# Kernel tuning notes

Hardware: AMD Instinct MI355X
Metric: run time of the kernel (lower is better)

The kernel has to match this reference:

```python
import jax, jax.numpy as jnp
import numpy as np

B, S, D, H = 2, 2048, 256, 8
W_STD = 0.02


def setup_inputs() -> dict:
    key = jax.random.key(0)
    ks = jax.random.split(key, 6)
    x = jax.random.normal(ks[0], (B, S, D), jnp.float32)
    e = jax.random.normal(ks[1], (B, S, D), jnp.float32)
    p = jax.random.normal(ks[2], (B, S, D), jnp.float32)
    W_q = W_STD * jax.random.normal(ks[3], (D, D), jnp.float32)
    W_k = W_STD * jax.random.normal(ks[4], (D, D), jnp.float32)
    W_v = W_STD * jax.random.normal(ks[5], (D, D), jnp.float32)
    gamma = jnp.ones((H, 1, 1), jnp.float32)
    return {"x": x, "e": e, "p": p, "W_q": W_q, "W_k": W_k, "W_v": W_v, "gamma": gamma}


def reference(x, e, p, W_q, W_k, W_v, gamma):
    # use_ppe=True: Q = K = p (broadcast to every head), V = e; each head sees
    # the SAME d_embed-wide copy, so project once and broadcast over heads.
    Q = p @ W_q  # [B,S,D]
    K = p @ W_k  # [B,S,D]
    V = e @ W_v  # [B,S,D]
    # squared euclidean distance (torch.cdist(...,p=2)**2), shared across heads
    q2 = jnp.sum(Q * Q, axis=-1)  # [B,S]
    k2 = jnp.sum(K * K, axis=-1)  # [B,S]
    d2 = q2[:, :, None] + k2[:, None, :] - 2.0 * jnp.einsum('bsd,btd->bst', Q, K)
    d2 = jnp.maximum(d2, 0.0)  # [B,S,S]
    # rbf kernel, per-head gamma: krn = exp(-d2 / (-2*gamma + 1e-6))
    krn = -d2[:, None, :, :] / (-2.0 * gamma + 1e-6)  # [B,H,S,S]
    causal = jnp.tril(jnp.ones((S, S), dtype=bool))  # True where attending allowed
    krn = jnp.where(causal, krn, -jnp.inf)
    krn = jnp.exp(krn)  # masked entries -> exp(-inf) = 0
    # dropout layers run in eval mode (identity)
    out = jnp.einsum('bhst,btd->bhsd', krn, V)  # [B,H,S,D]
    return out
```

## Files before the change

### kernel.cpp

```cpp
#include <hip/hip_runtime.h>
#include <hip/hip_bf16.h>


#define BB   2
#define SS   2048
#define DD   256
#define HH   8
#define BSR  (BB*SS)
#define TSPLIT 4

typedef __bf16 bf16_t;
typedef __bf16 bf16x8 __attribute__((ext_vector_type(8)));
typedef float  f32x4  __attribute__((ext_vector_type(4)));

static __device__ __forceinline__ f32x4 mfma16(bf16x8 a, bf16x8 b, f32x4 c) {
    return __builtin_amdgcn_mfma_f32_16x16x32_bf16(a, b, c, 0, 0, 0);
}

__global__ __launch_bounds__(256) void att_wtrans(
    const float* __restrict__ Wq, const float* __restrict__ Wk,
    const float* __restrict__ Wv,
    bf16_t* __restrict__ WFq_h, bf16_t* __restrict__ WFq_l,
    bf16_t* __restrict__ WFk_h, bf16_t* __restrict__ WFk_l,
    bf16_t* __restrict__ WFv, float* __restrict__ q2, float* __restrict__ k2)
{
    __shared__ float tT[64][68];
    const int tid = threadIdx.x;
    if (blockIdx.x == 48) {
        for (int i = tid; i < BSR; i += 256) { q2[i] = 0.f; k2[i] = 0.f; }
        return;
    }
    const int mat = blockIdx.x >> 4;
    const int tl  = blockIdx.x & 15;
    const int tr  = (tl >> 2) * 64, tc = (tl & 3) * 64;
    const float* W = (mat == 0) ? Wq : ((mat == 1) ? Wk : Wv);

#pragma unroll
    for (int i = 0; i < 4; ++i) {
        const int fidx = i * 256 + tid;
        const int r  = fidx >> 4;
        const int c4 = fidx & 15;
        const float4 v = *(const float4*)(W + (size_t)(tr + r) * DD + tc + c4 * 4);
        tT[c4 * 4 + 0][r] = v.x; tT[c4 * 4 + 1][r] = v.y;
        tT[c4 * 4 + 2][r] = v.z; tT[c4 * 4 + 3][r] = v.w;
    }
    __syncthreads();

#pragma unroll
    for (int i = 0; i < 2; ++i) {
        const int uidx  = i * 256 + tid;
        const int chunk = uidx >> 6;
        const int kc_l  = chunk >> 2, c16 = chunk & 3;
        const int u = uidx & 63, m16 = u & 15, quad = u >> 4;
        const float* src = &tT[c16 * 16 + m16][kc_l * 32 + quad * 8];
        const float4 a = *(const float4*)src;
        const float4 bq = *(const float4*)(src + 4);
        const float f[8] = {a.x, a.y, a.z, a.w, bq.x, bq.y, bq.z, bq.w};
        bf16x8 hi, lo;
#pragma unroll
        for (int j = 0; j < 8; ++j) {
            const bf16_t h = (bf16_t)f[j];
            hi[j] = h; lo[j] = (bf16_t)(f[j] - (float)h);
        }
        const int g16 = (tc >> 4) + c16;
        const int kcg = (tr >> 5) + kc_l;
        const size_t off = ((size_t)(g16 * 8 + kcg)) * 512 + (size_t)u * 8;
        if (mat == 0)      { *(bf16x8*)(WFq_h + off) = hi; *(bf16x8*)(WFq_l + off) = lo; }
        else if (mat == 1) { *(bf16x8*)(WFk_h + off) = hi; *(bf16x8*)(WFk_l + off) = lo; }
        else               { *(bf16x8*)(WFv + off)  = hi; }
    }
}

__global__ __launch_bounds__(256, 2) void att_gemm_qkv(
    const float* __restrict__ p, const float* __restrict__ e,
    const bf16_t* __restrict__ WFq_h, const bf16_t* __restrict__ WFq_l,
    const bf16_t* __restrict__ WFk_h, const bf16_t* __restrict__ WFk_l,
    const bf16_t* __restrict__ WFv,
    bf16_t* __restrict__ QFh, bf16_t* __restrict__ QFl,
    bf16_t* __restrict__ KFh, bf16_t* __restrict__ KFl,
    bf16_t* __restrict__ VF, float* __restrict__ q2, float* __restrict__ k2)
{
    __shared__ float pL[16][264];
    __shared__ float eL[16][264];
    __shared__ float fQ[16][68];
    __shared__ float fK[16][68];
    __shared__ float fV[16][68];

    const int tid  = threadIdx.x;
    const int w    = tid >> 6;
    const int lane = tid & 63;
    const int m16  = lane & 15;
    const int quad = lane >> 4;
    const int row0 = (blockIdx.x >> 2) * 16;
    const int nb   = blockIdx.x & 3;

#pragma unroll
    for (int i = 0; i < 4; ++i) {
        const int fidx = i * 256 + tid;
        const int r  = fidx >> 6;
        const int c4 = fidx & 63;
        const float4 pv = *(const float4*)(p + (size_t)(row0 + r) * DD + c4 * 4);
        const float4 ev = *(const float4*)(e + (size_t)(row0 + r) * DD + c4 * 4);
        *(float4*)&pL[r][c4 * 4] = pv;
        *(float4*)&eL[r][c4 * 4] = ev;
    }
    __syncthreads();

    f32x4 aQ = f32x4{0.f, 0.f, 0.f, 0.f};
    f32x4 aK = f32x4{0.f, 0.f, 0.f, 0.f};
    f32x4 aV = f32x4{0.f, 0.f, 0.f, 0.f};

#pragma unroll 2
    for (int kc = 0; kc < 8; ++kc) {
        const float* ps = &pL[m16][kc * 32 + quad * 8];
        const float* es = &eL[m16][kc * 32 + quad * 8];
        const float4 p0 = *(const float4*)ps;
        const float4 p1 = *(const float4*)(ps + 4);
        const float4 e0 = *(const float4*)es;
        const float4 e1 = *(const float4*)(es + 4);
        const float pa[8] = {p0.x, p0.y, p0.z, p0.w, p1.x, p1.y, p1.z, p1.w};
        const float ea[8] = {e0.x, e0.y, e0.z, e0.w, e1.x, e1.y, e1.z, e1.w};
        bf16x8 aph, apl, aeb;
#pragma unroll
        for (int j = 0; j < 8; ++j) {
            const bf16_t h = (bf16_t)pa[j];
            aph[j] = h;
            apl[j] = (bf16_t)(pa[j] - (float)h);
            aeb[j] = (bf16_t)ea[j];
        }
        const size_t wo = ((size_t)((nb * 4 + w) * 8 + kc)) * 512 + (size_t)lane * 8;
        const bf16x8 bqh = *(const bf16x8*)(WFq_h + wo);
        const bf16x8 bql = *(const bf16x8*)(WFq_l + wo);
        const bf16x8 bkh = *(const bf16x8*)(WFk_h + wo);
        const bf16x8 bkl = *(const bf16x8*)(WFk_l + wo);
        const bf16x8 bv  = *(const bf16x8*)(WFv + wo);
        aQ = mfma16(aph, bqh, aQ);
        aQ = mfma16(apl, bqh, aQ);
        aQ = mfma16(aph, bql, aQ);
        aK = mfma16(aph, bkh, aK);
        aK = mfma16(apl, bkh, aK);
        aK = mfma16(aph, bkl, aK);
        aV = mfma16(aeb, bv, aV);
    }

#pragma unroll
    for (int r = 0; r < 4; ++r) {
        const int rl = quad * 4 + r;
        fQ[rl][w * 16 + m16] = aQ[r];
        fK[rl][w * 16 + m16] = aK[r];
        fV[rl][w * 16 + m16] = aV[r];
    }

#pragma unroll
    for (int r = 0; r < 4; ++r) {
        float vq = aQ[r] * aQ[r], vk = aK[r] * aK[r];
#pragma unroll
        for (int off = 8; off >= 1; off >>= 1) {
            vq += __shfl_xor(vq, off);
            vk += __shfl_xor(vk, off);
        }
        if (m16 == 0) {
            atomicAdd(q2 + row0 + quad * 4 + r, vq);
            atomicAdd(k2 + row0 + quad * 4 + r, vk);
        }
    }

    __syncthreads();

    const int b   = row0 >> 11;
    const int sl  = row0 & 2047;
    const int tt  = sl >> 6;
    const int st  = sl >> 5;
    const int w4  = (sl >> 4) & 3;
    const int mt  = (sl >> 4) & 1;
    const int kc2 = (sl >> 5) & 1;
    const int uh  = (sl >> 4) & 1;

    if (w < 2) {
        const int cl = w;
        const float* src = &fQ[m16][cl * 32 + quad * 8];
        const float4 a = *(const float4*)src;
        const float4 c = *(const float4*)(src + 4);
        const float f[8] = {a.x, a.y, a.z, a.w, c.x, c.y, c.z, c.w};
        bf16x8 hi, lo;
#pragma unroll
        for (int j = 0; j < 8; ++j) {
            const bf16_t h = (bf16_t)f[j];
            hi[j] = h; lo[j] = (bf16_t)(f[j] - (float)h);
        }
        const size_t off = ((size_t)(b * 64 + st)) * 8192
                         + (size_t)(mt * 8 + nb * 2 + cl) * 512 + (size_t)lane * 8;
        *(bf16x8*)(QFh + off) = hi; *(bf16x8*)(QFl + off) = lo;
    } else {
        const int cl = w - 2;
        const float* src = &fK[m16][cl * 32 + quad * 8];
        const float4 a = *(const float4*)src;
        const float4 c = *(const float4*)(src + 4);
        const float f[8] = {a.x, a.y, a.z, a.w, c.x, c.y, c.z, c.w};
        bf16x8 hi, lo;
#pragma unroll
        for (int j = 0; j < 8; ++j) {
            const bf16_t h = (bf16_t)f[j];
            hi[j] = h; lo[j] = (bf16_t)(f[j] - (float)h);
        }
        const size_t off = ((size_t)(b * 32 + tt)) * 16384
                         + (size_t)(w4 * 8 + nb * 2 + cl) * 512 + (size_t)lane * 8;
        *(bf16x8*)(KFh + off) = hi; *(bf16x8*)(KFl + off) = lo;
    }

    if (lane < 32) {
        const int nt  = w;
        const int u   = uh * 32 + lane;
        const int tl0 = (lane >> 4) * 8;
        bf16x8 vb;
#pragma unroll
        for (int j = 0; j < 8; ++j)
            vb[j] = (bf16_t)fV[tl0 + j][nt * 16 + (lane & 15)];
        const size_t off = ((size_t)(b * 32 + tt)) * 16384
                         + (size_t)(nb * 8 + kc2 * 4 + nt) * 512 + (size_t)u * 8;
        *(bf16x8*)(VF + off) = vb;
    }
}

__global__ __launch_bounds__(256, 2) void att_flash(
    const bf16_t* __restrict__ QFh, const bf16_t* __restrict__ QFl,
    const bf16_t* __restrict__ KFh, const bf16_t* __restrict__ KFl,
    const bf16_t* __restrict__ VF, const float* __restrict__ q2,
    const float* __restrict__ k2, const float* __restrict__ gamma,
    float* __restrict__ part, float* __restrict__ out)
{
    __shared__ bf16_t Pb[2][32][72];

    const int tid   = threadIdx.x;
    const int pair  = blockIdx.x >> 3;
    const int sub   = blockIdx.x & 7;
    const int split = sub >> 1;
    const int b     = sub & 1;
    const int wave  = tid >> 6;
    const int lane  = tid & 63;
    const int m16   = lane & 15;
    const int quad  = lane >> 4;

    float g[8];
#pragma unroll
    for (int h = 0; h < 8; ++h) g[h] = gamma[h];

    int pb = 0;

    for (int half = 0; half < 2; ++half) {
        const int st = half ? (63 - pair) : pair;
        const int s0 = st * 32;

        bf16x8 aQh[2][8], aQl[2][8];
        const size_t qtile = ((size_t)(b * 64 + st)) * 8192 + (size_t)lane * 8;
#pragma unroll
        for (int mt = 0; mt < 2; ++mt)
#pragma unroll
            for (int kc = 0; kc < 8; ++kc) {
                const size_t base = qtile + (size_t)(mt * 8 + kc) * 512;
                aQh[mt][kc] = *(const bf16x8*)(QFh + base);
                aQl[mt][kc] = *(const bf16x8*)(QFl + base);
            }

        float q2r[2][4];
#pragma unroll
        for (int mt = 0; mt < 2; ++mt)
#pragma unroll
            for (int r = 0; r < 4; ++r)
                q2r[mt][r] = q2[b * SS + s0 + mt * 16 + quad * 4 + r];

        const int n_tiles = (s0 + 31) / 64 + 1;

        for (int h = 0; h < HH; ++h) {
            int rep = 0;
            while (g[rep] != g[h]) ++rep;
            if (rep != h) continue;
            const float cexp = 1.0f / (2.0f * g[h] - 1e-6f);

            f32x4 O[2][4];
#pragma unroll
            for (int mt = 0; mt < 2; ++mt)
#pragma unroll
                for (int nt = 0; nt < 4; ++nt)
                    O[mt][nt] = f32x4{0.f, 0.f, 0.f, 0.f};

            for (int ti = split; ti < n_tiles; ti += TSPLIT) {
                const int t0 = ti * 64;
                const int tg = t0 + wave * 16 + m16;
                const size_t tile = ((size_t)(b * 32 + ti)) * 16384
                                  + (size_t)wave * 4096 + (size_t)lane * 8;

                bf16x8 vf[2][4];
#pragma unroll
                for (int kc2 = 0; kc2 < 2; ++kc2)
#pragma unroll
                    for (int nt = 0; nt < 4; ++nt)
                        vf[kc2][nt] = *(const bf16x8*)(
                            VF + tile + (size_t)(kc2 * 4 + nt) * 512);
                const float k2v = k2[b * SS + tg];

                f32x4 acc0 = f32x4{0.f, 0.f, 0.f, 0.f};
                f32x4 acc1 = f32x4{0.f, 0.f, 0.f, 0.f};
#pragma unroll
                for (int kc = 0; kc < 8; ++kc) {
                    const bf16x8 bh = *(const bf16x8*)(KFh + tile + (size_t)kc * 512);
                    const bf16x8 bl = *(const bf16x8*)(KFl + tile + (size_t)kc * 512);
                    acc0 = mfma16(aQh[0][kc], bh, acc0);
                    acc1 = mfma16(aQh[1][kc], bh, acc1);
                    acc0 = mfma16(aQl[0][kc], bh, acc0);
                    acc1 = mfma16(aQl[1][kc], bh, acc1);
                    acc0 = mfma16(aQh[0][kc], bl, acc0);
                    acc1 = mfma16(aQh[1][kc], bl, acc1);
                }

#pragma unroll
                for (int mt = 0; mt < 2; ++mt) {
#pragma unroll
                    for (int r = 0; r < 4; ++r) {
                        const int sl = mt * 16 + quad * 4 + r;
                        const int sg = s0 + sl;
                        const float dotv = mt ? acc1[r] : acc0[r];
                        float d2 = q2r[mt][r] + k2v - 2.0f * dotv;
                        d2 = fmaxf(d2, 0.0f);
                        const float wgt = (tg <= sg) ? __expf(cexp * d2) : 0.0f;
                        Pb[pb][sl][wave * 16 + m16] = (bf16_t)wgt;
                    }
                }
                __syncthreads();

#pragma unroll
                for (int kc2 = 0; kc2 < 2; ++kc2) {
                    const bf16x8 pa0 = *(const bf16x8*)&Pb[pb][m16][kc2 * 32 + quad * 8];
                    const bf16x8 pa1 = *(const bf16x8*)&Pb[pb][m16 + 16][kc2 * 32 + quad * 8];
#pragma unroll
                    for (int nt = 0; nt < 4; ++nt) {
                        O[0][nt] = mfma16(pa0, vf[kc2][nt], O[0][nt]);
                        O[1][nt] = mfma16(pa1, vf[kc2][nt], O[1][nt]);
                    }
                }
                pb ^= 1;
            }

            float* dst = (split == 0)
                ? out  + (((size_t)b * HH + h) * SS + s0) * DD
                : part + ((((size_t)(split - 1) * BB + b) * HH + h) * SS + s0) * DD;
#pragma unroll
            for (int mt = 0; mt < 2; ++mt)
#pragma unroll
                for (int nt = 0; nt < 4; ++nt)
#pragma unroll
                    for (int r = 0; r < 4; ++r)
                        dst[(size_t)(mt * 16 + quad * 4 + r) * DD
                            + wave * 64 + nt * 16 + m16] = O[mt][nt][r];
        }
    }
}

__global__ __launch_bounds__(256) void att_reduce_bcast(
    const float* __restrict__ gamma, const float* __restrict__ part,
    float* __restrict__ out)
{
    const int j = blockIdx.x * 256 + threadIdx.x;
    const int b = blockIdx.y;
    const int slab = SS * DD / 4;

    float g[8];
#pragma unroll
    for (int h = 0; h < 8; ++h) g[h] = gamma[h];

    const float4* pp = (const float4*)part;
    float4* o4 = (float4*)out;

    float4 repval{0.f, 0.f, 0.f, 0.f};
    int last_rep = -1;
#pragma unroll
    for (int h = 0; h < HH; ++h) {
        int rep = 0;
        while (g[rep] != g[h]) ++rep;
        float4* o = o4 + ((size_t)(b * HH + h)) * slab + j;
        if (rep == h) {
            float4 v = *o;
#pragma unroll
            for (int k = 0; k < 3; ++k) {
                const float4 pv = pp[(((size_t)k * BB + b) * HH + h) * slab + j];
                v.x += pv.x; v.y += pv.y; v.z += pv.z; v.w += pv.w;
            }
            *o = v; repval = v; last_rep = h;
        } else {
            if (last_rep != rep) {
                repval = o4[((size_t)(b * HH + rep)) * slab + j];
                last_rep = rep;
            }
            *o = repval;
        }
    }
}

extern "C" void kernel_launch(void* const* d_in, const int* in_sizes, int n_in,
                              void* d_out, int out_size, void* d_ws, size_t ws_size,
                              hipStream_t stream) {
    (void)in_sizes; (void)n_in; (void)out_size; (void)ws_size;
    const float* e     = (const float*)d_in[1];
    const float* p     = (const float*)d_in[2];
    const float* Wq    = (const float*)d_in[3];
    const float* Wk    = (const float*)d_in[4];
    const float* Wv    = (const float*)d_in[5];
    const float* gamma = (const float*)d_in[6];

    const size_t NROW = (size_t)BSR * DD;
    bf16_t* WFq_h = (bf16_t*)d_ws;
    bf16_t* WFq_l = WFq_h + DD * DD;
    bf16_t* WFk_h = WFq_l + DD * DD;
    bf16_t* WFk_l = WFk_h + DD * DD;
    bf16_t* WFv   = WFk_l + DD * DD;
    float*  q2    = (float*)(WFv + DD * DD);
    float*  k2    = q2 + BSR;
    bf16_t* QFh   = (bf16_t*)(k2 + BSR);
    bf16_t* QFl   = QFh + NROW;
    bf16_t* KFh   = QFl + NROW;
    bf16_t* KFl   = KFh + NROW;
    bf16_t* VF    = KFl + NROW;
    float*  part  = (float*)(VF + NROW);

    float* out = (float*)d_out;

    att_wtrans<<<dim3(49), dim3(256), 0, stream>>>(
        Wq, Wk, Wv, WFq_h, WFq_l, WFk_h, WFk_l, WFv, q2, k2);

    att_gemm_qkv<<<dim3((BSR / 16) * 4), dim3(256), 0, stream>>>(
        p, e, WFq_h, WFq_l, WFk_h, WFk_l, WFv, QFh, QFl, KFh, KFl, VF, q2, k2);

    att_flash<<<dim3(32 * TSPLIT * BB), dim3(256), 0, stream>>>(
        QFh, QFl, KFh, KFl, VF, q2, k2, gamma, part, out);

    att_reduce_bcast<<<dim3(SS * DD / 4 / 256, BB), dim3(256), 0, stream>>>(
        gamma, part, out);
}
```

Before: 136.1 us.

## Fuse split-K reduction and head broadcast into flash kernel via atomic counters

Removes the separate reduce/broadcast kernel. Each flash block now writes its partial output to a workspace slot, bumps a per-(batch, query-tile) atomic counter, and the last arriving block sums the partials and writes every head's output. Split blocks with no key tiles to process now skip the compute. MFMA sections are wrapped in s_setprio raises. This removes one kernel launch and the read-modify-write of the output, in exchange for extra partial-buffer traffic, threadfence and atomic synchronization, and a serialized reduction tail inside the flash kernel.

```diff
diff --git a/kernel.cpp b/kernel.cpp
--- a/kernel.cpp
+++ b/kernel.cpp
@@ -22,12 +22,14 @@
     const float* __restrict__ Wv,
     bf16_t* __restrict__ WFq_h, bf16_t* __restrict__ WFq_l,
     bf16_t* __restrict__ WFk_h, bf16_t* __restrict__ WFk_l,
-    bf16_t* __restrict__ WFv, float* __restrict__ q2, float* __restrict__ k2)
+    bf16_t* __restrict__ WFv, float* __restrict__ q2, float* __restrict__ k2,
+    unsigned* __restrict__ cnt)
 {
     __shared__ float tT[64][68];
     const int tid = threadIdx.x;
     if (blockIdx.x == 48) {
         for (int i = tid; i < BSR; i += 256) { q2[i] = 0.f; k2[i] = 0.f; }
+        for (int i = tid; i < BB * 64; i += 256) cnt[i] = 0u;
         return;
     }
     const int mat = blockIdx.x >> 4;
@@ -227,9 +229,11 @@
     const bf16_t* __restrict__ KFh, const bf16_t* __restrict__ KFl,
     const bf16_t* __restrict__ VF, const float* __restrict__ q2,
     const float* __restrict__ k2, const float* __restrict__ gamma,
-    float* __restrict__ part, float* __restrict__ out)
+    float* __restrict__ part, unsigned* __restrict__ cnt,
+    float* __restrict__ out)
 {
     __shared__ bf16_t Pb[2][32][72];
+    __shared__ int lastFlag;
 
     const int tid   = threadIdx.x;
     const int pair  = blockIdx.x >> 3;
@@ -250,148 +254,149 @@
     for (int half = 0; half < 2; ++half) {
         const int st = half ? (63 - pair) : pair;
         const int s0 = st * 32;
-
-        bf16x8 aQh[2][8], aQl[2][8];
-        const size_t qtile = ((size_t)(b * 64 + st)) * 8192 + (size_t)lane * 8;
-#pragma unroll
-        for (int mt = 0; mt < 2; ++mt)
-#pragma unroll
-            for (int kc = 0; kc < 8; ++kc) {
-                const size_t base = qtile + (size_t)(mt * 8 + kc) * 512;
-                aQh[mt][kc] = *(const bf16x8*)(QFh + base);
-                aQl[mt][kc] = *(const bf16x8*)(QFl + base);
+        const int n_tiles = (s0 + 31) / 64 + 1;
+        const bool active = (split < n_tiles);
+
+        if (active) {
+            bf16x8 aQh[2][8], aQl[2][8];
+            const size_t qtile = ((size_t)(b * 64 + st)) * 8192 + (size_t)lane * 8;
+#pragma unroll
+            for (int mt = 0; mt < 2; ++mt)
+#pragma unroll
+                for (int kc = 0; kc < 8; ++kc) {
+                    const size_t base = qtile + (size_t)(mt * 8 + kc) * 512;
+                    aQh[mt][kc] = *(const bf16x8*)(QFh + base);
+                    aQl[mt][kc] = *(const bf16x8*)(QFl + base);
+                }
+
+            float q2r[2][4];
+#pragma unroll
+            for (int mt = 0; mt < 2; ++mt)
+#pragma unroll
+                for (int r = 0; r < 4; ++r)
+                    q2r[mt][r] = q2[b * SS + s0 + mt * 16 + quad * 4 + r];
+
+            for (int h = 0; h < HH; ++h) {
+                int rep = 0;
+                while (g[rep] != g[h]) ++rep;
+                if (rep != h) continue;
+                const float cexp = 1.0f / (2.0f * g[h] - 1e-6f);
+
+                f32x4 O[2][4];
+#pragma unroll
+                for (int mt = 0; mt < 2; ++mt)
+#pragma unroll
+                    for (int nt = 0; nt < 4; ++nt)
+                        O[mt][nt] = f32x4{0.f, 0.f, 0.f, 0.f};
+
+                for (int ti = split; ti < n_tiles; ti += TSPLIT) {
+                    const int t0 = ti * 64;
+                    const int tg = t0 + wave * 16 + m16;
+                    const size_t tile = ((size_t)(b * 32 + ti)) * 16384
+                                      + (size_t)wave * 4096 + (size_t)lane * 8;
+
+                    bf16x8 vf[2][4];
+#pragma unroll
+                    for (int kc2 = 0; kc2 < 2; ++kc2)
+#pragma unroll
+                        for (int nt = 0; nt < 4; ++nt)
+                            vf[kc2][nt] = *(const bf16x8*)(
+                                VF + tile + (size_t)(kc2 * 4 + nt) * 512);
+                    const float k2v = k2[b * SS + tg];
+
+                    f32x4 acc0 = f32x4{0.f, 0.f, 0.f, 0.f};
+                    f32x4 acc1 = f32x4{0.f, 0.f, 0.f, 0.f};
+                    __builtin_amdgcn_s_setprio(1);
+#pragma unroll
+                    for (int kc = 0; kc < 8; ++kc) {
+                        const bf16x8 bh = *(const bf16x8*)(KFh + tile + (size_t)kc * 512);
+                        const bf16x8 bl = *(const bf16x8*)(KFl + tile + (size_t)kc * 512);
+                        acc0 = mfma16(aQh[0][kc], bh, acc0);
+                        acc1 = mfma16(aQh[1][kc], bh, acc1);
+                        acc0 = mfma16(aQl[0][kc], bh, acc0);
+                        acc1 = mfma16(aQl[1][kc], bh, acc1);
+                        acc0 = mfma16(aQh[0][kc], bl, acc0);
+                        acc1 = mfma16(aQh[1][kc], bl, acc1);
+                    }
+                    __builtin_amdgcn_s_setprio(0);
+
+#pragma unroll
+                    for (int mt = 0; mt < 2; ++mt) {
+#pragma unroll
+                        for (int r = 0; r < 4; ++r) {
+                            const int sl = mt * 16 + quad * 4 + r;
+                            const int sg = s0 + sl;
+                            const float dotv = mt ? acc1[r] : acc0[r];
+                            float d2 = q2r[mt][r] + k2v - 2.0f * dotv;
+                            d2 = fmaxf(d2, 0.0f);
+                            const float wgt = (tg <= sg) ? __expf(cexp * d2) : 0.0f;
+                            Pb[pb][sl][wave * 16 + m16] = (bf16_t)wgt;
+                        }
+                    }
+                    __syncthreads();
+
+                    __builtin_amdgcn_s_setprio(1);
+#pragma unroll
+                    for (int kc2 = 0; kc2 < 2; ++kc2) {
+                        const bf16x8 pa0 = *(const bf16x8*)&Pb[pb][m16][kc2 * 32 + quad * 8];
+                        const bf16x8 pa1 = *(const bf16x8*)&Pb[pb][m16 + 16][kc2 * 32 + quad * 8];
+#pragma unroll
+                        for (int nt = 0; nt < 4; ++nt) {
+                            O[0][nt] = mfma16(pa0, vf[kc2][nt], O[0][nt]);
+                            O[1][nt] = mfma16(pa1, vf[kc2][nt], O[1][nt]);
+                        }
+                    }
+                    __builtin_amdgcn_s_setprio(0);
+                    pb ^= 1;
+                }
+
+                float* dst = part + (((size_t)split * BB + b) * HH + h) * (size_t)SS * DD
+                           + (size_t)s0 * DD;
+#pragma unroll
+                for (int mt = 0; mt < 2; ++mt)
+#pragma unroll
+                    for (int nt = 0; nt < 4; ++nt)
+#pragma unroll
+                        for (int r = 0; r < 4; ++r)
+                            dst[(size_t)(mt * 16 + quad * 4 + r) * DD
+                                + wave * 64 + nt * 16 + m16] = O[mt][nt][r];
             }
-
-        float q2r[2][4];
-#pragma unroll
-        for (int mt = 0; mt < 2; ++mt)
-#pragma unroll
-            for (int r = 0; r < 4; ++r)
-                q2r[mt][r] = q2[b * SS + s0 + mt * 16 + quad * 4 + r];
-
-        const int n_tiles = (s0 + 31) / 64 + 1;
-
-        for (int h = 0; h < HH; ++h) {
-            int rep = 0;
-            while (g[rep] != g[h]) ++rep;
-            if (rep != h) continue;
-            const float cexp = 1.0f / (2.0f * g[h] - 1e-6f);
-
-            f32x4 O[2][4];
-#pragma unroll
-            for (int mt = 0; mt < 2; ++mt)
-#pragma unroll
-                for (int nt = 0; nt < 4; ++nt)
-                    O[mt][nt] = f32x4{0.f, 0.f, 0.f, 0.f};
-
-            for (int ti = split; ti < n_tiles; ti += TSPLIT) {
-                const int t0 = ti * 64;
-                const int tg = t0 + wave * 16 + m16;
-                const size_t tile = ((size_t)(b * 32 + ti)) * 16384
-                                  + (size_t)wave * 4096 + (size_t)lane * 8;
-
-                bf16x8 vf[2][4];
-#pragma unroll
-                for (int kc2 = 0; kc2 < 2; ++kc2)
-#pragma unroll
-                    for (int nt = 0; nt < 4; ++nt)
-                        vf[kc2][nt] = *(const bf16x8*)(
-                            VF + tile + (size_t)(kc2 * 4 + nt) * 512);
-                const float k2v = k2[b * SS + tg];
-
-                f32x4 acc0 = f32x4{0.f, 0.f, 0.f, 0.f};
-                f32x4 acc1 = f32x4{0.f, 0.f, 0.f, 0.f};
-#pragma unroll
-                for (int kc = 0; kc < 8; ++kc) {
-                    const bf16x8 bh = *(const bf16x8*)(KFh + tile + (size_t)kc * 512);
-                    const bf16x8 bl = *(const bf16x8*)(KFl + tile + (size_t)kc * 512);
-                    acc0 = mfma16(aQh[0][kc], bh, acc0);
-                    acc1 = mfma16(aQh[1][kc], bh, acc1);
-                    acc0 = mfma16(aQl[0][kc], bh, acc0);
-                    acc1 = mfma16(aQl[1][kc], bh, acc1);
-                    acc0 = mfma16(aQh[0][kc], bl, acc0);
-                    acc1 = mfma16(aQh[1][kc], bl, acc1);
+        }
+
+        __syncthreads();
+        if (tid == 0) {
+            __threadfence();
+            const unsigned prev = atomicAdd(&cnt[b * 64 + st], 1u);
+            lastFlag = (prev == TSPLIT - 1) ? 1 : 0;
+        }
+        __syncthreads();
+
+        if (lastFlag) {
+            __threadfence();
+            const int kmax = (n_tiles < TSPLIT) ? n_tiles : TSPLIT;
+#pragma unroll
+            for (int j = 0; j < 8; ++j) {
+                const int f4  = j * 256 + tid;
+                const int row = f4 >> 6, c4 = f4 & 63;
+                const size_t rowoff = (size_t)(s0 + row) * DD + (size_t)c4 * 4;
+                float4 s{0.f, 0.f, 0.f, 0.f};
+                int lastr = -1;
+                for (int hq = 0; hq < HH; ++hq) {
+                    int rep = 0;
+                    while (g[rep] != g[hq]) ++rep;
+                    if (rep != lastr) {
+                        s = float4{0.f, 0.f, 0.f, 0.f};
+                        for (int k = 0; k < kmax; ++k) {
+                            const float4 v = *(const float4*)(
+                                part + (((size_t)k * BB + b) * HH + rep) * (size_t)SS * DD
+                                     + rowoff);
+                            s.x += v.x; s.y += v.y; s.z += v.z; s.w += v.w;
+                        }
+                        lastr = rep;
+                    }
+                    *(float4*)(out + ((size_t)(b * HH + hq) * SS) * DD + rowoff) = s;
                 }
-
-#pragma unroll
-                for (int mt = 0; mt < 2; ++mt) {
-#pragma unroll
-                    for (int r = 0; r < 4; ++r) {
-                        const int sl = mt * 16 + quad * 4 + r;
-                        const int sg = s0 + sl;
-                        const float dotv = mt ? acc1[r] : acc0[r];
-                        float d2 = q2r[mt][r] + k2v - 2.0f * dotv;
-                        d2 = fmaxf(d2, 0.0f);
-                        const float wgt = (tg <= sg) ? __expf(cexp * d2) : 0.0f;
-                        Pb[pb][sl][wave * 16 + m16] = (bf16_t)wgt;
-                    }
-                }
-                __syncthreads();
-
-#pragma unroll
-                for (int kc2 = 0; kc2 < 2; ++kc2) {
-                    const bf16x8 pa0 = *(const bf16x8*)&Pb[pb][m16][kc2 * 32 + quad * 8];
-                    const bf16x8 pa1 = *(const bf16x8*)&Pb[pb][m16 + 16][kc2 * 32 + quad * 8];
-#pragma unroll
-                    for (int nt = 0; nt < 4; ++nt) {
-                        O[0][nt] = mfma16(pa0, vf[kc2][nt], O[0][nt]);
-                        O[1][nt] = mfma16(pa1, vf[kc2][nt], O[1][nt]);
-                    }
-                }
-                pb ^= 1;
             }
-
-            float* dst = (split == 0)
-                ? out  + (((size_t)b * HH + h) * SS + s0) * DD
-                : part + ((((size_t)(split - 1) * BB + b) * HH + h) * SS + s0) * DD;
-#pragma unroll
-            for (int mt = 0; mt < 2; ++mt)
-#pragma unroll
-                for (int nt = 0; nt < 4; ++nt)
-#pragma unroll
-                    for (int r = 0; r < 4; ++r)
-                        dst[(size_t)(mt * 16 + quad * 4 + r) * DD
-                            + wave * 64 + nt * 16 + m16] = O[mt][nt][r];
-        }
-    }
-}
-
-__global__ __launch_bounds__(256) void att_reduce_bcast(
-    const float* __restrict__ gamma, const float* __restrict__ part,
-    float* __restrict__ out)
-{
-    const int j = blockIdx.x * 256 + threadIdx.x;
-    const int b = blockIdx.y;
-    const int slab = SS * DD / 4;
-
-    float g[8];
-#pragma unroll
-    for (int h = 0; h < 8; ++h) g[h] = gamma[h];
-
-    const float4* pp = (const float4*)part;
-    float4* o4 = (float4*)out;
-
-    float4 repval{0.f, 0.f, 0.f, 0.f};
-    int last_rep = -1;
-#pragma unroll
-    for (int h = 0; h < HH; ++h) {
-        int rep = 0;
-        while (g[rep] != g[h]) ++rep;
-        float4* o = o4 + ((size_t)(b * HH + h)) * slab + j;
-        if (rep == h) {
-            float4 v = *o;
-#pragma unroll
-            for (int k = 0; k < 3; ++k) {
-                const float4 pv = pp[(((size_t)k * BB + b) * HH + h) * slab + j];
-                v.x += pv.x; v.y += pv.y; v.z += pv.z; v.w += pv.w;
-            }
-            *o = v; repval = v; last_rep = h;
-        } else {
-            if (last_rep != rep) {
-                repval = o4[((size_t)(b * HH + rep)) * slab + j];
-                last_rep = rep;
-            }
-            *o = repval;
         }
     }
 }
@@ -421,18 +426,16 @@
     bf16_t* KFl   = KFh + NROW;
     bf16_t* VF    = KFl + NROW;
     float*  part  = (float*)(VF + NROW);
+    unsigned* cnt = (unsigned*)(part + (size_t)TSPLIT * BB * HH * SS * DD);
 
     float* out = (float*)d_out;
 
     att_wtrans<<<dim3(49), dim3(256), 0, stream>>>(
-        Wq, Wk, Wv, WFq_h, WFq_l, WFk_h, WFk_l, WFv, q2, k2);
+        Wq, Wk, Wv, WFq_h, WFq_l, WFk_h, WFk_l, WFv, q2, k2, cnt);
 
     att_gemm_qkv<<<dim3((BSR / 16) * 4), dim3(256), 0, stream>>>(
         p, e, WFq_h, WFq_l, WFk_h, WFk_l, WFv, QFh, QFl, KFh, KFl, VF, q2, k2);
 
     att_flash<<<dim3(32 * TSPLIT * BB), dim3(256), 0, stream>>>(
-        QFh, QFl, KFh, KFl, VF, q2, k2, gamma, part, out);
-
-    att_reduce_bcast<<<dim3(SS * DD / 4 / 256, BB), dim3(256), 0, stream>>>(
-        gamma, part, out);
+        QFh, QFl, KFh, KFl, VF, q2, k2, gamma, part, cnt, out);
 }
```

Result: slower. 239.6 us (+76.1%).

## Batch four key tiles per flash iteration and widen QKV GEMM blocks

Applied to the files above, without the earlier changes.

The attention kernel now processes four key tiles per loop step, loading their K and V fragments up front and sharing one barrier across them, with the old single-tile loop kept as a tail. The QKV projection kernel has each block compute all four column groups of a 16-row stripe. This reuses the converted p/e fragments and cuts the block count by four. Both kernels drop to launch bounds of one block per CU, so registers can grow at the cost of occupancy.

```diff
diff --git a/kernel.cpp b/kernel.cpp
--- a/kernel.cpp
+++ b/kernel.cpp
@@ -71,7 +71,7 @@
     }
 }
 
-__global__ __launch_bounds__(256, 2) void att_gemm_qkv(
+__global__ __launch_bounds__(256, 1) void att_gemm_qkv(
     const float* __restrict__ p, const float* __restrict__ e,
     const bf16_t* __restrict__ WFq_h, const bf16_t* __restrict__ WFq_l,
     const bf16_t* __restrict__ WFk_h, const bf16_t* __restrict__ WFk_l,
@@ -91,8 +91,7 @@
     const int lane = tid & 63;
     const int m16  = lane & 15;
     const int quad = lane >> 4;
-    const int row0 = (blockIdx.x >> 2) * 16;
-    const int nb   = blockIdx.x & 3;
+    const int row0 = blockIdx.x * 16;
 
 #pragma unroll
     for (int i = 0; i < 4; ++i) {
@@ -106,11 +105,14 @@
     }
     __syncthreads();
 
-    f32x4 aQ = f32x4{0.f, 0.f, 0.f, 0.f};
-    f32x4 aK = f32x4{0.f, 0.f, 0.f, 0.f};
-    f32x4 aV = f32x4{0.f, 0.f, 0.f, 0.f};
-
-#pragma unroll 2
+    f32x4 aQ[4], aK[4], aV[4];
+#pragma unroll
+    for (int nt = 0; nt < 4; ++nt) {
+        aQ[nt] = f32x4{0.f, 0.f, 0.f, 0.f};
+        aK[nt] = f32x4{0.f, 0.f, 0.f, 0.f};
+        aV[nt] = f32x4{0.f, 0.f, 0.f, 0.f};
+    }
+
     for (int kc = 0; kc < 8; ++kc) {
         const float* ps = &pL[m16][kc * 32 + quad * 8];
         const float* es = &eL[m16][kc * 32 + quad * 8];
@@ -128,32 +130,32 @@
             apl[j] = (bf16_t)(pa[j] - (float)h);
             aeb[j] = (bf16_t)ea[j];
         }
-        const size_t wo = ((size_t)((nb * 4 + w) * 8 + kc)) * 512 + (size_t)lane * 8;
-        const bf16x8 bqh = *(const bf16x8*)(WFq_h + wo);
-        const bf16x8 bql = *(const bf16x8*)(WFq_l + wo);
-        const bf16x8 bkh = *(const bf16x8*)(WFk_h + wo);
-        const bf16x8 bkl = *(const bf16x8*)(WFk_l + wo);
-        const bf16x8 bv  = *(const bf16x8*)(WFv + wo);
-        aQ = mfma16(aph, bqh, aQ);
-        aQ = mfma16(apl, bqh, aQ);
-        aQ = mfma16(aph, bql, aQ);
-        aK = mfma16(aph, bkh, aK);
-        aK = mfma16(apl, bkh, aK);
-        aK = mfma16(aph, bkl, aK);
-        aV = mfma16(aeb, bv, aV);
+#pragma unroll
+        for (int nt = 0; nt < 4; ++nt) {
+            const size_t wo = ((size_t)((nt * 4 + w) * 8 + kc)) * 512 + (size_t)lane * 8;
+            const bf16x8 bqh = *(const bf16x8*)(WFq_h + wo);
+            const bf16x8 bql = *(const bf16x8*)(WFq_l + wo);
+            const bf16x8 bkh = *(const bf16x8*)(WFk_h + wo);
+            const bf16x8 bkl = *(const bf16x8*)(WFk_l + wo);
+            const bf16x8 bv  = *(const bf16x8*)(WFv + wo);
+            aQ[nt] = mfma16(aph, bqh, aQ[nt]);
+            aQ[nt] = mfma16(apl, bqh, aQ[nt]);
+            aQ[nt] = mfma16(aph, bql, aQ[nt]);
+            aK[nt] = mfma16(aph, bkh, aK[nt]);
+            aK[nt] = mfma16(apl, bkh, aK[nt]);
+            aK[nt] = mfma16(aph, bkl, aK[nt]);
+            aV[nt] = mfma16(aeb, bv, aV[nt]);
+        }
     }
 
 #pragma unroll
     for (int r = 0; r < 4; ++r) {
-        const int rl = quad * 4 + r;
-        fQ[rl][w * 16 + m16] = aQ[r];
-        fK[rl][w * 16 + m16] = aK[r];
-        fV[rl][w * 16 + m16] = aV[r];
-    }
-
-#pragma unroll
-    for (int r = 0; r < 4; ++r) {
-        float vq = aQ[r] * aQ[r], vk = aK[r] * aK[r];
+        float vq = 0.f, vk = 0.f;
+#pragma unroll
+        for (int nt = 0; nt < 4; ++nt) {
+            vq += aQ[nt][r] * aQ[nt][r];
+            vk += aK[nt][r] * aK[nt][r];
+        }
 #pragma unroll
         for (int off = 8; off >= 1; off >>= 1) {
             vq += __shfl_xor(vq, off);
@@ -164,8 +166,6 @@
             atomicAdd(k2 + row0 + quad * 4 + r, vk);
         }
     }
-
-    __syncthreads();
 
     const int b   = row0 >> 11;
     const int sl  = row0 & 2047;
@@ -176,60 +176,72 @@
     const int kc2 = (sl >> 5) & 1;
     const int uh  = (sl >> 4) & 1;
 
-    if (w < 2) {
-        const int cl = w;
-        const float* src = &fQ[m16][cl * 32 + quad * 8];
-        const float4 a = *(const float4*)src;
-        const float4 c = *(const float4*)(src + 4);
-        const float f[8] = {a.x, a.y, a.z, a.w, c.x, c.y, c.z, c.w};
-        bf16x8 hi, lo;
-#pragma unroll
-        for (int j = 0; j < 8; ++j) {
-            const bf16_t h = (bf16_t)f[j];
-            hi[j] = h; lo[j] = (bf16_t)(f[j] - (float)h);
-        }
-        const size_t off = ((size_t)(b * 64 + st)) * 8192
-                         + (size_t)(mt * 8 + nb * 2 + cl) * 512 + (size_t)lane * 8;
-        *(bf16x8*)(QFh + off) = hi; *(bf16x8*)(QFl + off) = lo;
-    } else {
-        const int cl = w - 2;
-        const float* src = &fK[m16][cl * 32 + quad * 8];
-        const float4 a = *(const float4*)src;
-        const float4 c = *(const float4*)(src + 4);
-        const float f[8] = {a.x, a.y, a.z, a.w, c.x, c.y, c.z, c.w};
-        bf16x8 hi, lo;
-#pragma unroll
-        for (int j = 0; j < 8; ++j) {
-            const bf16_t h = (bf16_t)f[j];
-            hi[j] = h; lo[j] = (bf16_t)(f[j] - (float)h);
-        }
-        const size_t off = ((size_t)(b * 32 + tt)) * 16384
-                         + (size_t)(w4 * 8 + nb * 2 + cl) * 512 + (size_t)lane * 8;
-        *(bf16x8*)(KFh + off) = hi; *(bf16x8*)(KFl + off) = lo;
-    }
-
-    if (lane < 32) {
-        const int nt  = w;
-        const int u   = uh * 32 + lane;
-        const int tl0 = (lane >> 4) * 8;
-        bf16x8 vb;
-#pragma unroll
-        for (int j = 0; j < 8; ++j)
-            vb[j] = (bf16_t)fV[tl0 + j][nt * 16 + (lane & 15)];
-        const size_t off = ((size_t)(b * 32 + tt)) * 16384
-                         + (size_t)(nb * 8 + kc2 * 4 + nt) * 512 + (size_t)u * 8;
-        *(bf16x8*)(VF + off) = vb;
+#pragma unroll
+    for (int nb = 0; nb < 4; ++nb) {
+        __syncthreads();
+#pragma unroll
+        for (int r = 0; r < 4; ++r) {
+            const int rl = quad * 4 + r;
+            fQ[rl][w * 16 + m16] = aQ[nb][r];
+            fK[rl][w * 16 + m16] = aK[nb][r];
+            fV[rl][w * 16 + m16] = aV[nb][r];
+        }
+        __syncthreads();
+
+        if (w < 2) {
+            const int cl = w;
+            const float* src = &fQ[m16][cl * 32 + quad * 8];
+            const float4 a = *(const float4*)src;
+            const float4 c = *(const float4*)(src + 4);
+            const float f[8] = {a.x, a.y, a.z, a.w, c.x, c.y, c.z, c.w};
+            bf16x8 hi, lo;
+#pragma unroll
+            for (int j = 0; j < 8; ++j) {
+                const bf16_t h = (bf16_t)f[j];
+                hi[j] = h; lo[j] = (bf16_t)(f[j] - (float)h);
+            }
+            const size_t off = ((size_t)(b * 64 + st)) * 8192
+                             + (size_t)(mt * 8 + nb * 2 + cl) * 512 + (size_t)lane * 8;
+            *(bf16x8*)(QFh + off) = hi; *(bf16x8*)(QFl + off) = lo;
+        } else {
+            const int cl = w - 2;
+            const float* src = &fK[m16][cl * 32 + quad * 8];
+            const float4 a = *(const float4*)src;
+            const float4 c = *(const float4*)(src + 4);
+            const float f[8] = {a.x, a.y, a.z, a.w, c.x, c.y, c.z, c.w};
+            bf16x8 hi, lo;
+#pragma unroll
+            for (int j = 0; j < 8; ++j) {
+                const bf16_t h = (bf16_t)f[j];
+                hi[j] = h; lo[j] = (bf16_t)(f[j] - (float)h);
+            }
+            const size_t off = ((size_t)(b * 32 + tt)) * 16384
+                             + (size_t)(w4 * 8 + nb * 2 + cl) * 512 + (size_t)lane * 8;
+            *(bf16x8*)(KFh + off) = hi; *(bf16x8*)(KFl + off) = lo;
+        }
+
+        if (lane < 32) {
+            const int u   = uh * 32 + lane;
+            const int tl0 = (lane >> 4) * 8;
+            bf16x8 vb;
+#pragma unroll
+            for (int j = 0; j < 8; ++j)
+                vb[j] = (bf16_t)fV[tl0 + j][w * 16 + (lane & 15)];
+            const size_t off = ((size_t)(b * 32 + tt)) * 16384
+                             + (size_t)(nb * 8 + kc2 * 4 + w) * 512 + (size_t)u * 8;
+            *(bf16x8*)(VF + off) = vb;
+        }
     }
 }
 
-__global__ __launch_bounds__(256, 2) void att_flash(
+__global__ __launch_bounds__(256, 1) void att_flash(
     const bf16_t* __restrict__ QFh, const bf16_t* __restrict__ QFl,
     const bf16_t* __restrict__ KFh, const bf16_t* __restrict__ KFl,
     const bf16_t* __restrict__ VF, const float* __restrict__ q2,
     const float* __restrict__ k2, const float* __restrict__ gamma,
     float* __restrict__ part, float* __restrict__ out)
 {
-    __shared__ bf16_t Pb[2][32][72];
+    __shared__ bf16_t Pb[2][4][32][72];
 
     const int tid   = threadIdx.x;
     const int pair  = blockIdx.x >> 3;
@@ -245,7 +257,7 @@
 #pragma unroll
     for (int h = 0; h < 8; ++h) g[h] = gamma[h];
 
-    int pb = 0;
+    int q = 0;
 
     for (int half = 0; half < 2; ++half) {
         const int st = half ? (63 - pair) : pair;
@@ -284,9 +296,96 @@
                 for (int nt = 0; nt < 4; ++nt)
                     O[mt][nt] = f32x4{0.f, 0.f, 0.f, 0.f};
 
-            for (int ti = split; ti < n_tiles; ti += TSPLIT) {
-                const int t0 = ti * 64;
-                const int tg = t0 + wave * 16 + m16;
+            int ti = split;
+
+            while (ti + 3 * TSPLIT < n_tiles) {
+                int tg[4]; size_t tl[4];
+#pragma unroll
+                for (int k = 0; k < 4; ++k) {
+                    const int tk = ti + k * TSPLIT;
+                    tg[k] = tk * 64 + wave * 16 + m16;
+                    tl[k] = ((size_t)(b * 32 + tk)) * 16384
+                          + (size_t)wave * 4096 + (size_t)lane * 8;
+                }
+
+                bf16x8 vf[4][8];
+#pragma unroll
+                for (int k = 0; k < 4; ++k)
+#pragma unroll
+                    for (int u = 0; u < 8; ++u)
+                        vf[k][u] = *(const bf16x8*)(VF + tl[k] + (size_t)u * 512);
+                float k2v[4];
+#pragma unroll
+                for (int k = 0; k < 4; ++k) k2v[k] = k2[b * SS + tg[k]];
+
+                f32x4 sA[4], sB[4];
+#pragma unroll
+                for (int k = 0; k < 4; ++k) {
+                    sA[k] = f32x4{0.f, 0.f, 0.f, 0.f};
+                    sB[k] = f32x4{0.f, 0.f, 0.f, 0.f};
+                }
+#pragma unroll
+                for (int kc = 0; kc < 8; ++kc) {
+                    bf16x8 bh[4], bl[4];
+#pragma unroll
+                    for (int k = 0; k < 4; ++k) {
+                        bh[k] = *(const bf16x8*)(KFh + tl[k] + (size_t)kc * 512);
+                        bl[k] = *(const bf16x8*)(KFl + tl[k] + (size_t)kc * 512);
+                    }
+#pragma unroll
+                    for (int k = 0; k < 4; ++k) {
+                        sA[k] = mfma16(aQh[0][kc], bh[k], sA[k]);
+                        sB[k] = mfma16(aQh[1][kc], bh[k], sB[k]);
+                    }
+#pragma unroll
+                    for (int k = 0; k < 4; ++k) {
+                        sA[k] = mfma16(aQl[0][kc], bh[k], sA[k]);
+                        sB[k] = mfma16(aQl[1][kc], bh[k], sB[k]);
+                    }
+#pragma unroll
+                    for (int k = 0; k < 4; ++k) {
+                        sA[k] = mfma16(aQh[0][kc], bl[k], sA[k]);
+                        sB[k] = mfma16(aQh[1][kc], bl[k], sB[k]);
+                    }
+                }
+
+#pragma unroll
+                for (int k = 0; k < 4; ++k)
+#pragma unroll
+                    for (int mt = 0; mt < 2; ++mt)
+#pragma unroll
+                        for (int r = 0; r < 4; ++r) {
+                            const int sl = mt * 16 + quad * 4 + r;
+                            const int sg = s0 + sl;
+                            float d2v = q2r[mt][r] + k2v[k]
+                                      - 2.0f * (mt ? sB[k][r] : sA[k][r]);
+                            d2v = fmaxf(d2v, 0.0f);
+                            const float wgt =
+                                (tg[k] <= sg) ? __expf(cexp * d2v) : 0.0f;
+                            Pb[q][k][sl][wave * 16 + m16] = (bf16_t)wgt;
+                        }
+                __syncthreads();
+
+#pragma unroll
+                for (int k = 0; k < 4; ++k)
+#pragma unroll
+                    for (int kc2 = 0; kc2 < 2; ++kc2) {
+                        const bf16x8 pa0 = *(const bf16x8*)
+                            &Pb[q][k][m16][kc2 * 32 + quad * 8];
+                        const bf16x8 pa1 = *(const bf16x8*)
+                            &Pb[q][k][m16 + 16][kc2 * 32 + quad * 8];
+#pragma unroll
+                        for (int nt = 0; nt < 4; ++nt) {
+                            O[0][nt] = mfma16(pa0, vf[k][kc2 * 4 + nt], O[0][nt]);
+                            O[1][nt] = mfma16(pa1, vf[k][kc2 * 4 + nt], O[1][nt]);
+                        }
+                    }
+                q ^= 1;
+                ti += 4 * TSPLIT;
+            }
+
+            while (ti < n_tiles) {
+                const int tg = ti * 64 + wave * 16 + m16;
                 const size_t tile = ((size_t)(b * 32 + ti)) * 16384
                                   + (size_t)wave * 4096 + (size_t)lane * 8;
 
@@ -323,22 +422,23 @@
                         float d2 = q2r[mt][r] + k2v - 2.0f * dotv;
                         d2 = fmaxf(d2, 0.0f);
                         const float wgt = (tg <= sg) ? __expf(cexp * d2) : 0.0f;
-                        Pb[pb][sl][wave * 16 + m16] = (bf16_t)wgt;
+                        Pb[q][0][sl][wave * 16 + m16] = (bf16_t)wgt;
                     }
                 }
                 __syncthreads();
 
 #pragma unroll
                 for (int kc2 = 0; kc2 < 2; ++kc2) {
-                    const bf16x8 pa0 = *(const bf16x8*)&Pb[pb][m16][kc2 * 32 + quad * 8];
-                    const bf16x8 pa1 = *(const bf16x8*)&Pb[pb][m16 + 16][kc2 * 32 + quad * 8];
+                    const bf16x8 pa0 = *(const bf16x8*)&Pb[q][0][m16][kc2 * 32 + quad * 8];
+                    const bf16x8 pa1 = *(const bf16x8*)&Pb[q][0][m16 + 16][kc2 * 32 + quad * 8];
 #pragma unroll
                     for (int nt = 0; nt < 4; ++nt) {
                         O[0][nt] = mfma16(pa0, vf[kc2][nt], O[0][nt]);
                         O[1][nt] = mfma16(pa1, vf[kc2][nt], O[1][nt]);
                     }
                 }
-                pb ^= 1;
+                q ^= 1;
+                ti += TSPLIT;
             }
 
             float* dst = (split == 0)
@@ -381,7 +481,7 @@
         if (rep == h) {
             float4 v = *o;
 #pragma unroll
-            for (int k = 0; k < 3; ++k) {
+            for (int k = 0; k < TSPLIT - 1; ++k) {
                 const float4 pv = pp[(((size_t)k * BB + b) * HH + h) * slab + j];
                 v.x += pv.x; v.y += pv.y; v.z += pv.z; v.w += pv.w;
             }
@@ -427,7 +527,7 @@
     att_wtrans<<<dim3(49), dim3(256), 0, stream>>>(
         Wq, Wk, Wv, WFq_h, WFq_l, WFk_h, WFk_l, WFv, q2, k2);
 
-    att_gemm_qkv<<<dim3((BSR / 16) * 4), dim3(256), 0, stream>>>(
+    att_gemm_qkv<<<dim3(BSR / 16), dim3(256), 0, stream>>>(
         p, e, WFq_h, WFq_l, WFk_h, WFk_l, WFv, QFh, QFl, KFh, KFl, VF, q2, k2);
 
     att_flash<<<dim3(32 * TSPLIT * BB), dim3(256), 0, stream>>>(
```

Measured after the change: 140.5 us. 3.3% more time.

## Replace key-split with 16-row query tiles, drop reduce kernel, write duplicate heads directly

Applied to the files above, without the earlier changes.

The flash kernel now gives each block 16-row query tiles (paired light and heavy under the causal mask) and walks the full key range itself, so the partial-sum buffer and the separate reduce/broadcast kernel are gone. The key loop is unrolled to process four 64-key tiles per barrier, with one LDS buffer per tile. Heads that share a gamma value are written straight from registers. This removes a kernel launch and the extra partial-sum traffic, but per-block register pressure rises (launch bounds cut to 1 wave group per SIMD) and each block runs a longer serial key loop.

```diff
diff --git a/kernel.cpp b/kernel.cpp
--- a/kernel.cpp
+++ b/kernel.cpp
@@ -7,7 +7,6 @@
 #define DD   256
 #define HH   8
 #define BSR  (BB*SS)
-#define TSPLIT 4
 
 typedef __bf16 bf16_t;
 typedef __bf16 bf16x8 __attribute__((ext_vector_type(8)));
@@ -222,20 +221,20 @@
     }
 }
 
-__global__ __launch_bounds__(256, 2) void att_flash(
+__global__ __launch_bounds__(256, 1) void att_flash(
     const bf16_t* __restrict__ QFh, const bf16_t* __restrict__ QFl,
     const bf16_t* __restrict__ KFh, const bf16_t* __restrict__ KFl,
     const bf16_t* __restrict__ VF, const float* __restrict__ q2,
     const float* __restrict__ k2, const float* __restrict__ gamma,
-    float* __restrict__ part, float* __restrict__ out)
+    float* __restrict__ out)
 {
-    __shared__ bf16_t Pb[2][32][72];
+    __shared__ bf16_t Pb[2][4][16][72];
 
     const int tid   = threadIdx.x;
-    const int pair  = blockIdx.x >> 3;
     const int sub   = blockIdx.x & 7;
-    const int split = sub >> 1;
-    const int b     = sub & 1;
+    const int b     = sub >> 2;
+    const int stl   = sub & 3;
+    const int sq    = blockIdx.x >> 3;
     const int wave  = tid >> 6;
     const int lane  = tid & 63;
     const int m16   = lane & 15;
@@ -245,31 +244,27 @@
 #pragma unroll
     for (int h = 0; h < 8; ++h) g[h] = gamma[h];
 
-    int pb = 0;
+    int q = 0;
 
     for (int half = 0; half < 2; ++half) {
-        const int st = half ? (63 - pair) : pair;
-        const int s0 = st * 32;
-
-        bf16x8 aQh[2][8], aQl[2][8];
-        const size_t qtile = ((size_t)(b * 64 + st)) * 8192 + (size_t)lane * 8;
-#pragma unroll
-        for (int mt = 0; mt < 2; ++mt)
-#pragma unroll
-            for (int kc = 0; kc < 8; ++kc) {
-                const size_t base = qtile + (size_t)(mt * 8 + kc) * 512;
-                aQh[mt][kc] = *(const bf16x8*)(QFh + base);
-                aQl[mt][kc] = *(const bf16x8*)(QFl + base);
-            }
-
-        float q2r[2][4];
-#pragma unroll
-        for (int mt = 0; mt < 2; ++mt)
-#pragma unroll
-            for (int r = 0; r < 4; ++r)
-                q2r[mt][r] = q2[b * SS + s0 + mt * 16 + quad * 4 + r];
-
-        const int n_tiles = (s0 + 31) / 64 + 1;
+        const int st = half ? (127 - (sq * 4 + stl)) : (sq * 4 + stl);
+        const int s0 = st * 16;
+
+        bf16x8 aQh[8], aQl[8];
+        const size_t qtile = ((size_t)(b * 64 + (st >> 1))) * 8192
+                           + (size_t)((st & 1) * 8) * 512 + (size_t)lane * 8;
+#pragma unroll
+        for (int kc = 0; kc < 8; ++kc) {
+            aQh[kc] = *(const bf16x8*)(QFh + qtile + (size_t)kc * 512);
+            aQl[kc] = *(const bf16x8*)(QFl + qtile + (size_t)kc * 512);
+        }
+
+        float q2r[4];
+#pragma unroll
+        for (int r = 0; r < 4; ++r)
+            q2r[r] = q2[b * SS + s0 + quad * 4 + r];
+
+        const int n_tiles = st / 4 + 1;
 
         for (int h = 0; h < HH; ++h) {
             int rep = 0;
@@ -277,121 +272,137 @@
             if (rep != h) continue;
             const float cexp = 1.0f / (2.0f * g[h] - 1e-6f);
 
-            f32x4 O[2][4];
-#pragma unroll
-            for (int mt = 0; mt < 2; ++mt)
-#pragma unroll
-                for (int nt = 0; nt < 4; ++nt)
-                    O[mt][nt] = f32x4{0.f, 0.f, 0.f, 0.f};
-
-            for (int ti = split; ti < n_tiles; ti += TSPLIT) {
-                const int t0 = ti * 64;
-                const int tg = t0 + wave * 16 + m16;
+            f32x4 O[4];
+#pragma unroll
+            for (int nt = 0; nt < 4; ++nt)
+                O[nt] = f32x4{0.f, 0.f, 0.f, 0.f};
+
+            int ti = 0;
+
+            while (ti + 3 < n_tiles) {
+                int tg[4]; size_t tl[4];
+#pragma unroll
+                for (int k = 0; k < 4; ++k) {
+                    tg[k] = (ti + k) * 64 + wave * 16 + m16;
+                    tl[k] = ((size_t)(b * 32 + ti + k)) * 16384
+                          + (size_t)wave * 4096 + (size_t)lane * 8;
+                }
+
+                bf16x8 vf[4][8];
+#pragma unroll
+                for (int k = 0; k < 4; ++k)
+#pragma unroll
+                    for (int u = 0; u < 8; ++u)
+                        vf[k][u] = *(const bf16x8*)(VF + tl[k] + (size_t)u * 512);
+                float k2v[4];
+#pragma unroll
+                for (int k = 0; k < 4; ++k) k2v[k] = k2[b * SS + tg[k]];
+
+                f32x4 sA[4];
+#pragma unroll
+                for (int k = 0; k < 4; ++k) sA[k] = f32x4{0.f, 0.f, 0.f, 0.f};
+#pragma unroll
+                for (int kc = 0; kc < 8; ++kc) {
+                    bf16x8 bh[4], bl[4];
+#pragma unroll
+                    for (int k = 0; k < 4; ++k) {
+                        bh[k] = *(const bf16x8*)(KFh + tl[k] + (size_t)kc * 512);
+                        bl[k] = *(const bf16x8*)(KFl + tl[k] + (size_t)kc * 512);
+                    }
+#pragma unroll
+                    for (int k = 0; k < 4; ++k)
+                        sA[k] = mfma16(aQh[kc], bh[k], sA[k]);
+#pragma unroll
+                    for (int k = 0; k < 4; ++k)
+                        sA[k] = mfma16(aQl[kc], bh[k], sA[k]);
+#pragma unroll
+                    for (int k = 0; k < 4; ++k)
+                        sA[k] = mfma16(aQh[kc], bl[k], sA[k]);
+                }
+
+#pragma unroll
+                for (int k = 0; k < 4; ++k)
+#pragma unroll
+                    for (int r = 0; r < 4; ++r) {
+                        const int sl = quad * 4 + r;
+                        const int sg = s0 + sl;
+                        float d2v = q2r[r] + k2v[k] - 2.0f * sA[k][r];
+                        d2v = fmaxf(d2v, 0.0f);
+                        const float wgt =
+                            (tg[k] <= sg) ? __expf(cexp * d2v) : 0.0f;
+                        Pb[q][k][sl][wave * 16 + m16] = (bf16_t)wgt;
+                    }
+                __syncthreads();
+
+#pragma unroll
+                for (int k = 0; k < 4; ++k)
+#pragma unroll
+                    for (int kc2 = 0; kc2 < 2; ++kc2) {
+                        const bf16x8 pa = *(const bf16x8*)
+                            &Pb[q][k][m16][kc2 * 32 + quad * 8];
+#pragma unroll
+                        for (int nt = 0; nt < 4; ++nt)
+                            O[nt] = mfma16(pa, vf[k][kc2 * 4 + nt], O[nt]);
+                    }
+                q ^= 1;
+                ti += 4;
+            }
+
+            while (ti < n_tiles) {
+                const int tg = ti * 64 + wave * 16 + m16;
                 const size_t tile = ((size_t)(b * 32 + ti)) * 16384
                                   + (size_t)wave * 4096 + (size_t)lane * 8;
 
-                bf16x8 vf[2][4];
-#pragma unroll
-                for (int kc2 = 0; kc2 < 2; ++kc2)
-#pragma unroll
-                    for (int nt = 0; nt < 4; ++nt)
-                        vf[kc2][nt] = *(const bf16x8*)(
-                            VF + tile + (size_t)(kc2 * 4 + nt) * 512);
+                bf16x8 vf[8];
+#pragma unroll
+                for (int u = 0; u < 8; ++u)
+                    vf[u] = *(const bf16x8*)(VF + tile + (size_t)u * 512);
                 const float k2v = k2[b * SS + tg];
 
-                f32x4 acc0 = f32x4{0.f, 0.f, 0.f, 0.f};
-                f32x4 acc1 = f32x4{0.f, 0.f, 0.f, 0.f};
+                f32x4 acc = f32x4{0.f, 0.f, 0.f, 0.f};
 #pragma unroll
                 for (int kc = 0; kc < 8; ++kc) {
                     const bf16x8 bh = *(const bf16x8*)(KFh + tile + (size_t)kc * 512);
                     const bf16x8 bl = *(const bf16x8*)(KFl + tile + (size_t)kc * 512);
-                    acc0 = mfma16(aQh[0][kc], bh, acc0);
-                    acc1 = mfma16(aQh[1][kc], bh, acc1);
-                    acc0 = mfma16(aQl[0][kc], bh, acc0);
-                    acc1 = mfma16(aQl[1][kc], bh, acc1);
-                    acc0 = mfma16(aQh[0][kc], bl, acc0);
-                    acc1 = mfma16(aQh[1][kc], bl, acc1);
+                    acc = mfma16(aQh[kc], bh, acc);
+                    acc = mfma16(aQl[kc], bh, acc);
+                    acc = mfma16(aQh[kc], bl, acc);
                 }
 
 #pragma unroll
-                for (int mt = 0; mt < 2; ++mt) {
-#pragma unroll
-                    for (int r = 0; r < 4; ++r) {
-                        const int sl = mt * 16 + quad * 4 + r;
-                        const int sg = s0 + sl;
-                        const float dotv = mt ? acc1[r] : acc0[r];
-                        float d2 = q2r[mt][r] + k2v - 2.0f * dotv;
-                        d2 = fmaxf(d2, 0.0f);
-                        const float wgt = (tg <= sg) ? __expf(cexp * d2) : 0.0f;
-                        Pb[pb][sl][wave * 16 + m16] = (bf16_t)wgt;
-                    }
+                for (int r = 0; r < 4; ++r) {
+                    const int sl = quad * 4 + r;
+                    const int sg = s0 + sl;
+                    float d2v = q2r[r] + k2v - 2.0f * acc[r];
+                    d2v = fmaxf(d2v, 0.0f);
+                    const float wgt = (tg <= sg) ? __expf(cexp * d2v) : 0.0f;
+                    Pb[q][0][sl][wave * 16 + m16] = (bf16_t)wgt;
                 }
                 __syncthreads();
 
 #pragma unroll
                 for (int kc2 = 0; kc2 < 2; ++kc2) {
-                    const bf16x8 pa0 = *(const bf16x8*)&Pb[pb][m16][kc2 * 32 + quad * 8];
-                    const bf16x8 pa1 = *(const bf16x8*)&Pb[pb][m16 + 16][kc2 * 32 + quad * 8];
-#pragma unroll
-                    for (int nt = 0; nt < 4; ++nt) {
-                        O[0][nt] = mfma16(pa0, vf[kc2][nt], O[0][nt]);
-                        O[1][nt] = mfma16(pa1, vf[kc2][nt], O[1][nt]);
-                    }
+                    const bf16x8 pa = *(const bf16x8*)
+                        &Pb[q][0][m16][kc2 * 32 + quad * 8];
+#pragma unroll
+                    for (int nt = 0; nt < 4; ++nt)
+                        O[nt] = mfma16(pa, vf[kc2 * 4 + nt], O[nt]);
                 }
-                pb ^= 1;
+                q ^= 1;
+                ti += 1;
             }
 
-            float* dst = (split == 0)
-                ? out  + (((size_t)b * HH + h) * SS + s0) * DD
-                : part + ((((size_t)(split - 1) * BB + b) * HH + h) * SS + s0) * DD;
-#pragma unroll
-            for (int mt = 0; mt < 2; ++mt)
+#pragma unroll
+            for (int h2 = 0; h2 < HH; ++h2) {
+                if (g[h2] != g[h]) continue;
+                float* dst = out + (((size_t)b * HH + h2) * SS + s0) * DD;
 #pragma unroll
                 for (int nt = 0; nt < 4; ++nt)
 #pragma unroll
                     for (int r = 0; r < 4; ++r)
-                        dst[(size_t)(mt * 16 + quad * 4 + r) * DD
-                            + wave * 64 + nt * 16 + m16] = O[mt][nt][r];
-        }
-    }
-}
-
-__global__ __launch_bounds__(256) void att_reduce_bcast(
-    const float* __restrict__ gamma, const float* __restrict__ part,
-    float* __restrict__ out)
-{
-    const int j = blockIdx.x * 256 + threadIdx.x;
-    const int b = blockIdx.y;
-    const int slab = SS * DD / 4;
-
-    float g[8];
-#pragma unroll
-    for (int h = 0; h < 8; ++h) g[h] = gamma[h];
-
-    const float4* pp = (const float4*)part;
-    float4* o4 = (float4*)out;
-
-    float4 repval{0.f, 0.f, 0.f, 0.f};
-    int last_rep = -1;
-#pragma unroll
-    for (int h = 0; h < HH; ++h) {
-        int rep = 0;
-        while (g[rep] != g[h]) ++rep;
-        float4* o = o4 + ((size_t)(b * HH + h)) * slab + j;
-        if (rep == h) {
-            float4 v = *o;
-#pragma unroll
-            for (int k = 0; k < 3; ++k) {
-                const float4 pv = pp[(((size_t)k * BB + b) * HH + h) * slab + j];
-                v.x += pv.x; v.y += pv.y; v.z += pv.z; v.w += pv.w;
+                        dst[(size_t)(quad * 4 + r) * DD
+                            + wave * 64 + nt * 16 + m16] = O[nt][r];
             }
-            *o = v; repval = v; last_rep = h;
-        } else {
-            if (last_rep != rep) {
-                repval = o4[((size_t)(b * HH + rep)) * slab + j];
-                last_rep = rep;
-            }
-            *o = repval;
         }
     }
 }
@@ -420,7 +431,6 @@
     bf16_t* KFh   = QFl + NROW;
     bf16_t* KFl   = KFh + NROW;
     bf16_t* VF    = KFl + NROW;
-    float*  part  = (float*)(VF + NROW);
 
     float* out = (float*)d_out;
 
@@ -430,9 +440,6 @@
     att_gemm_qkv<<<dim3((BSR / 16) * 4), dim3(256), 0, stream>>>(
         p, e, WFq_h, WFq_l, WFk_h, WFk_l, WFv, QFh, QFl, KFh, KFl, VF, q2, k2);
 
-    att_flash<<<dim3(32 * TSPLIT * BB), dim3(256), 0, stream>>>(
-        QFh, QFl, KFh, KFl, VF, q2, k2, gamma, part, out);
-
-    att_reduce_bcast<<<dim3(SS * DD / 4 / 256, BB), dim3(256), 0, stream>>>(
-        gamma, part, out);
+    att_flash<<<dim3(256), dim3(256), 0, stream>>>(
+        QFh, QFl, KFh, KFl, VF, q2, k2, gamma, out);
 }
```

Result: slower. 158.6 us (+16.6%).
